# Performance work log

Measured on AMD Instinct MI355X. Metric: run time of the kernel, lower is better.

## Reference

```python
import jax, jax.numpy as jnp
import numpy as np

B, S, DIN, DOUT = 4, 4096, 4096, 4096
W_SCALE = 0.02  # kaiming-ish scale; keeps values inside fp8 range


def setup_inputs() -> dict:
    key = jax.random.key(0)
    k1, k2, k3 = jax.random.split(key, 3)
    x = jax.random.normal(k1, (B, S, DIN), dtype=jnp.float16)
    weight = (jax.random.normal(k2, (DOUT, DIN), dtype=jnp.float32) * W_SCALE).astype(jnp.float16)
    bias = (jax.random.normal(k3, (DOUT,), dtype=jnp.float32) * W_SCALE).astype(jnp.float16)
    return {"x": x, "weight": weight, "bias": bias}


def reference(x, weight, bias):
    # Emulate torch._scaled_mm: activations quantized to fp8 e5m2,
    # weight (transposed) quantized to fp8 e4m3fn, scale_a = scale_b = 1.0,
    # accumulate in fp32, add fp16 bias, output fp16.
    out_shape = x.shape[:-1] + (weight.shape[0],)
    x8 = x.reshape(-1, x.shape[-1]).astype(jnp.float8_e5m2)       # [M, DIN]
    w8 = weight.T.astype(jnp.float8_e4m3fn)                        # [DIN, DOUT]
    scale = jnp.float32(1.0)  # scale_a * scale_b
    acc = jnp.matmul(x8.astype(jnp.float32), w8.astype(jnp.float32))  # [M, DOUT] fp32 accum
    out = (acc * scale + bias.astype(jnp.float32)).astype(jnp.float16)
    return out.reshape(out_shape)
```

## Files before the change

### kernel.cpp

```cpp
#include <hip/hip_runtime.h>
#include <hip/hip_fp16.h>

#define M_DIM 16384
#define N_DIM 4096
#define K_DIM 4096

typedef __attribute__((ext_vector_type(16))) float f32x16;
typedef __attribute__((ext_vector_type(4)))  int   i32x4;
typedef __attribute__((ext_vector_type(8)))  int   i32x8;

template<bool E4M3>
__global__ __launch_bounds__(256) void quant_tile_kernel(
    const float* __restrict__ in,
    uint4* __restrict__ out,
    int ngrp)
{
  int t = blockIdx.x * 256 + threadIdx.x;
  if (t >= ngrp) return;
  const int g    = t & 1023;
  const int tile = t >> 10;
  const int kt   = tile & 63;
  const int bt   = tile >> 6;
  const int sb   = g >> 7;
  const int half = (g >> 6) & 1;
  const int l    = g & 63;
  const int row  = bt * 256 + sb * 32 + (l & 31);
  const int k    = kt * 64 + (l >> 5) * 32 + half * 16;

  const float4* p = reinterpret_cast<const float4*>(in + (size_t)row * K_DIM + k);
  float4 v0 = p[0], v1 = p[1], v2 = p[2], v3 = p[3];
  int w0 = 0, w1 = 0, w2 = 0, w3 = 0;
  if (E4M3) {
    w0 = __builtin_amdgcn_cvt_pk_fp8_f32(v0.x, v0.y, w0, false);
    w0 = __builtin_amdgcn_cvt_pk_fp8_f32(v0.z, v0.w, w0, true);
    w1 = __builtin_amdgcn_cvt_pk_fp8_f32(v1.x, v1.y, w1, false);
    w1 = __builtin_amdgcn_cvt_pk_fp8_f32(v1.z, v1.w, w1, true);
    w2 = __builtin_amdgcn_cvt_pk_fp8_f32(v2.x, v2.y, w2, false);
    w2 = __builtin_amdgcn_cvt_pk_fp8_f32(v2.z, v2.w, w2, true);
    w3 = __builtin_amdgcn_cvt_pk_fp8_f32(v3.x, v3.y, w3, false);
    w3 = __builtin_amdgcn_cvt_pk_fp8_f32(v3.z, v3.w, w3, true);
  } else {
    w0 = __builtin_amdgcn_cvt_pk_bf8_f32(v0.x, v0.y, w0, false);
    w0 = __builtin_amdgcn_cvt_pk_bf8_f32(v0.z, v0.w, w0, true);
    w1 = __builtin_amdgcn_cvt_pk_bf8_f32(v1.x, v1.y, w1, false);
    w1 = __builtin_amdgcn_cvt_pk_bf8_f32(v1.z, v1.w, w1, true);
    w2 = __builtin_amdgcn_cvt_pk_bf8_f32(v2.x, v2.y, w2, false);
    w2 = __builtin_amdgcn_cvt_pk_bf8_f32(v2.z, v2.w, w2, true);
    w3 = __builtin_amdgcn_cvt_pk_bf8_f32(v3.x, v3.y, w3, false);
    w3 = __builtin_amdgcn_cvt_pk_bf8_f32(v3.z, v3.w, w3, true);
  }
  out[t] = make_uint4((unsigned)w0, (unsigned)w1, (unsigned)w2, (unsigned)w3);
}

__global__ __launch_bounds__(512, 2) void gemm_fp8_kernel(
    const unsigned char* __restrict__ Aq,
    const unsigned char* __restrict__ Wq,
    const float* __restrict__ bias,
    float* __restrict__ C)
{
  __shared__ __align__(16) unsigned char lds[65536];

  const int tid  = threadIdx.x;
  const int lane = tid & 63;
  const int wave = tid >> 6;
  const int wr   = wave >> 2;
  const int wc   = wave & 3;

  const int bid = blockIdx.x;
  const int swz = (bid & 7) * 128 + (bid >> 3);
  const int bmi = swz >> 4;
  const int bni = swz & 15;

  const unsigned char* tA = Aq + (size_t)bmi * 64 * 16384;
  const unsigned char* tB = Wq + (size_t)bni * 64 * 16384;

  const size_t t16 = (size_t)tid * 16;
  const int    w1k = wave * 1024;

#define STAGE(gbase, ldsoff)                                                \
  __builtin_amdgcn_global_load_lds(                                         \
      (const __attribute__((address_space(1))) void*)((gbase) + t16),       \
      (__attribute__((address_space(3))) void*)(lds + (ldsoff) + w1k), 16, 0, 0)

#define RDFRAG(dst, byteoff)                                                \
  { const unsigned char* _p = lds + (byteoff) + lane * 16;                  \
    i32x4 _lo = *(const i32x4*)_p;                                          \
    i32x4 _hi = *(const i32x4*)(_p + 1024);                                 \
    dst = i32x8{_lo.x, _lo.y, _lo.z, _lo.w, _hi.x, _hi.y, _hi.z, _hi.w}; }

#define MFMA(d, a, b)                                                       \
  d = __builtin_amdgcn_mfma_scale_f32_32x32x64_f8f6f4(                      \
      a, b, d, 1 , 0 , 0, 0x7F7F7F7F, 0, 0x7F7F7F7F)

  const int aoff = wr * 8192;
  const int boff = 16384 + wc * 4096;

  f32x16 acc[4][2] = {};
  i32x8 aE0, aE1, aE2, aE3, bE0, bE1;
  i32x8 aO0, aO1, aO2, aO3, bO0, bO1;

  STAGE(tA,              0);
  STAGE(tA + 8192,       8192);
  STAGE(tB,              16384);
  STAGE(tB + 8192,       24576);
  __builtin_amdgcn_sched_barrier(0);
  STAGE(tA + 16384,          32768);
  STAGE(tA + 16384 + 8192,   40960);
  STAGE(tB + 16384,          49152);
  STAGE(tB + 16384 + 8192,   57344);
  __builtin_amdgcn_sched_barrier(0);
  asm volatile("s_waitcnt vmcnt(4)" ::: "memory");
  __builtin_amdgcn_s_barrier();
  RDFRAG(aE0, aoff + 0 * 2048);  RDFRAG(aE1, aoff + 1 * 2048);
  RDFRAG(aE2, aoff + 2 * 2048);  RDFRAG(aE3, aoff + 3 * 2048);
  RDFRAG(bE0, boff + 0 * 2048);  RDFRAG(bE1, boff + 1 * 2048);
  asm volatile("s_waitcnt lgkmcnt(0)" ::: "memory");
  __builtin_amdgcn_sched_barrier(0);
  __builtin_amdgcn_s_barrier();

  for (int kt = 0; kt < 64; kt += 2) {
    {
      const size_t tp = (size_t)((kt + 2) & 63) * 16384;
      STAGE(tA + tp,        0);
      STAGE(tA + tp + 8192, 8192);
      STAGE(tB + tp,        16384);
      STAGE(tB + tp + 8192, 24576);
      asm volatile("s_waitcnt vmcnt(4)" ::: "memory");
      __builtin_amdgcn_s_barrier();
      RDFRAG(aO0, 32768 + aoff + 0 * 2048);
      RDFRAG(aO1, 32768 + aoff + 1 * 2048);
      RDFRAG(aO2, 32768 + aoff + 2 * 2048);
      RDFRAG(aO3, 32768 + aoff + 3 * 2048);
      RDFRAG(bO0, 32768 + boff + 0 * 2048);
      RDFRAG(bO1, 32768 + boff + 1 * 2048);
      __builtin_amdgcn_s_setprio(1);
      MFMA(acc[0][0], aE0, bE0); MFMA(acc[0][1], aE0, bE1);
      MFMA(acc[1][0], aE1, bE0); MFMA(acc[1][1], aE1, bE1);
      MFMA(acc[2][0], aE2, bE0); MFMA(acc[2][1], aE2, bE1);
      MFMA(acc[3][0], aE3, bE0); MFMA(acc[3][1], aE3, bE1);
      __builtin_amdgcn_s_setprio(0);
      __builtin_amdgcn_sched_barrier(0);
      asm volatile("s_waitcnt lgkmcnt(0)" ::: "memory");
      __builtin_amdgcn_sched_barrier(0);
      __builtin_amdgcn_s_barrier();
    }
    {
      const size_t tp = (size_t)((kt + 3) & 63) * 16384;
      STAGE(tA + tp,        32768);
      STAGE(tA + tp + 8192, 40960);
      STAGE(tB + tp,        49152);
      STAGE(tB + tp + 8192, 57344);
      asm volatile("s_waitcnt vmcnt(4)" ::: "memory");
      __builtin_amdgcn_s_barrier();
      RDFRAG(aE0, aoff + 0 * 2048);
      RDFRAG(aE1, aoff + 1 * 2048);
      RDFRAG(aE2, aoff + 2 * 2048);
      RDFRAG(aE3, aoff + 3 * 2048);
      RDFRAG(bE0, boff + 0 * 2048);
      RDFRAG(bE1, boff + 1 * 2048);
      __builtin_amdgcn_s_setprio(1);
      MFMA(acc[0][0], aO0, bO0); MFMA(acc[0][1], aO0, bO1);
      MFMA(acc[1][0], aO1, bO0); MFMA(acc[1][1], aO1, bO1);
      MFMA(acc[2][0], aO2, bO0); MFMA(acc[2][1], aO2, bO1);
      MFMA(acc[3][0], aO3, bO0); MFMA(acc[3][1], aO3, bO1);
      __builtin_amdgcn_s_setprio(0);
      __builtin_amdgcn_sched_barrier(0);
      asm volatile("s_waitcnt lgkmcnt(0)" ::: "memory");
      __builtin_amdgcn_sched_barrier(0);
      __builtin_amdgcn_s_barrier();
    }
  }
#undef STAGE
#undef RDFRAG
#undef MFMA

  #pragma unroll
  for (int n = 0; n < 2; ++n) {
    const int col = bni * 256 + wc * 64 + n * 32 + (lane & 31);
    const float bv = bias[col];
    #pragma unroll
    for (int m = 0; m < 4; ++m) {
      const int rbase = bmi * 256 + wr * 128 + m * 32 + ((lane >> 5) << 2);
      #pragma unroll
      for (int r = 0; r < 16; ++r) {
        const int row = rbase + (r & 3) + 8 * (r >> 2);
        C[(size_t)row * N_DIM + col] =
            __half2float(__float2half_rn(acc[m][n][r] + bv));
      }
    }
  }
}

extern "C" void kernel_launch(void* const* d_in, const int* in_sizes, int n_in,
                              void* d_out, int out_size, void* d_ws, size_t ws_size,
                              hipStream_t stream) {
  const float* x  = (const float*)d_in[0];
  const float* w  = (const float*)d_in[1];
  const float* bs = (const float*)d_in[2];
  float* out = (float*)d_out;

  unsigned char* xq = (unsigned char*)d_ws;
  unsigned char* wq = (unsigned char*)d_ws + (size_t)M_DIM * K_DIM;

  const int ngx = (M_DIM * K_DIM) / 16;
  const int ngw = (N_DIM * K_DIM) / 16;
  quant_tile_kernel<false><<<ngx / 256, 256, 0, stream>>>(x, (uint4*)xq, ngx);
  quant_tile_kernel<true ><<<ngw / 256, 256, 0, stream>>>(w, (uint4*)wq, ngw);

  gemm_fp8_kernel<<<1024, 512, 0, stream>>>(xq, wq, bs, out);
}
```

Before: 358.2 us.

## Use 4 waves with 128x128 per-wave tiles and remap block order

Cuts the GEMM block from 8 waves to 4, so each wave computes a 128x128 sub-tile (4x4 MFMA accumulators) instead of 128x64. This raises register-level reuse of A/B fragments per LDS read. Each thread now issues 8 global-to-LDS loads per stage instead of 4. The block index mapping also changes so consecutive swizzled blocks walk along M within an N column rather than along N. The trade-off is fewer waves to hide latency and much higher register pressure (256 accumulator floats plus double-buffered fragments), with launch bounds of 1 block per CU.

```diff
diff --git a/kernel.cpp b/kernel.cpp
--- a/kernel.cpp
+++ b/kernel.cpp
@@ -52,7 +52,7 @@
   out[t] = make_uint4((unsigned)w0, (unsigned)w1, (unsigned)w2, (unsigned)w3);
 }
 
-__global__ __launch_bounds__(512, 2) void gemm_fp8_kernel(
+__global__ __launch_bounds__(256, 1) void gemm_fp8_kernel(
     const unsigned char* __restrict__ Aq,
     const unsigned char* __restrict__ Wq,
     const float* __restrict__ bias,
@@ -63,82 +63,94 @@
   const int tid  = threadIdx.x;
   const int lane = tid & 63;
   const int wave = tid >> 6;
-  const int wr   = wave >> 2;
-  const int wc   = wave & 3;
+  const int wr   = wave >> 1;
+  const int wc   = wave & 1;
 
   const int bid = blockIdx.x;
   const int swz = (bid & 7) * 128 + (bid >> 3);
-  const int bmi = swz >> 4;
-  const int bni = swz & 15;
-
-  const unsigned char* tA = Aq + (size_t)bmi * 64 * 16384;
-  const unsigned char* tB = Wq + (size_t)bni * 64 * 16384;
+  const int bni = swz >> 6;
+  const int bmi = swz & 63;
+
+  const unsigned char* tA = Aq + (size_t)bmi * (64 * 16384);
+  const unsigned char* tB = Wq + (size_t)bni * (64 * 16384);
 
   const size_t t16 = (size_t)tid * 16;
   const int    w1k = wave * 1024;
 
-#define STAGE(gbase, ldsoff)                                                \
-  __builtin_amdgcn_global_load_lds(                                         \
-      (const __attribute__((address_space(1))) void*)((gbase) + t16),       \
-      (__attribute__((address_space(3))) void*)(lds + (ldsoff) + w1k), 16, 0, 0)
-
-#define RDFRAG(dst, byteoff)                                                \
-  { const unsigned char* _p = lds + (byteoff) + lane * 16;                  \
-    i32x4 _lo = *(const i32x4*)_p;                                          \
-    i32x4 _hi = *(const i32x4*)(_p + 1024);                                 \
-    dst = i32x8{_lo.x, _lo.y, _lo.z, _lo.w, _hi.x, _hi.y, _hi.z, _hi.w}; }
-
-#define MFMA(d, a, b)                                                       \
-  d = __builtin_amdgcn_mfma_scale_f32_32x32x64_f8f6f4(                      \
-      a, b, d, 1 , 0 , 0, 0x7F7F7F7F, 0, 0x7F7F7F7F)
-
-  const int aoff = wr * 8192;
-  const int boff = 16384 + wc * 4096;
-
-  f32x16 acc[4][2] = {};
-  i32x8 aE0, aE1, aE2, aE3, bE0, bE1;
-  i32x8 aO0, aO1, aO2, aO3, bO0, bO1;
-
-  STAGE(tA,              0);
-  STAGE(tA + 8192,       8192);
-  STAGE(tB,              16384);
-  STAGE(tB + 8192,       24576);
+#define STAGE(gb, lo_)                                                      \
+  __builtin_amdgcn_global_load_lds(                                        \
+      (const __attribute__((address_space(1))) void*)((gb) + t16),          \
+      (__attribute__((address_space(3))) void*)(lds + (lo_) + w1k), 16, 0, 0)
+
+#define STAGE_TILE(tp, ldsbase)                                             \
+  STAGE(tA + (tp),         (ldsbase) + 0);                                  \
+  STAGE(tA + (tp) + 4096,  (ldsbase) + 4096);                               \
+  STAGE(tA + (tp) + 8192,  (ldsbase) + 8192);                               \
+  STAGE(tA + (tp) + 12288, (ldsbase) + 12288);                              \
+  STAGE(tB + (tp),         (ldsbase) + 16384);                              \
+  STAGE(tB + (tp) + 4096,  (ldsbase) + 20480);                              \
+  STAGE(tB + (tp) + 8192,  (ldsbase) + 24576);                              \
+  STAGE(tB + (tp) + 12288, (ldsbase) + 28672)
+
+#define RD(lo_, hi_, off)                                                   \
+  { const unsigned char* _p = lds + (off) + lane * 16;                      \
+    lo_ = *(const i32x4*)_p; hi_ = *(const i32x4*)(_p + 1024); }
+
+#define J(l_, h_) __builtin_shufflevector(l_, h_, 0, 1, 2, 3, 4, 5, 6, 7)
+
+  const int aoff = wr * 4 * 2048;
+  const int boff = 16384 + wc * 4 * 2048;
+
+  f32x16 acc[4][4] = {};
+  i32x4 aEl[4], aEh[4], bEl[4], bEh[4];
+  i32x4 aOl[4], aOh[4], bOl[4], bOh[4];
+
+  STAGE_TILE(0, 0);
   __builtin_amdgcn_sched_barrier(0);
-  STAGE(tA + 16384,          32768);
-  STAGE(tA + 16384 + 8192,   40960);
-  STAGE(tB + 16384,          49152);
-  STAGE(tB + 16384 + 8192,   57344);
+  STAGE_TILE(16384, 32768);
   __builtin_amdgcn_sched_barrier(0);
-  asm volatile("s_waitcnt vmcnt(4)" ::: "memory");
+  asm volatile("s_waitcnt vmcnt(8)" ::: "memory");
   __builtin_amdgcn_s_barrier();
-  RDFRAG(aE0, aoff + 0 * 2048);  RDFRAG(aE1, aoff + 1 * 2048);
-  RDFRAG(aE2, aoff + 2 * 2048);  RDFRAG(aE3, aoff + 3 * 2048);
-  RDFRAG(bE0, boff + 0 * 2048);  RDFRAG(bE1, boff + 1 * 2048);
+  #pragma unroll
+  for (int m = 0; m < 4; ++m) RD(aEl[m], aEh[m], aoff + m * 2048);
+  #pragma unroll
+  for (int n = 0; n < 4; ++n) RD(bEl[n], bEh[n], boff + n * 2048);
   asm volatile("s_waitcnt lgkmcnt(0)" ::: "memory");
   __builtin_amdgcn_sched_barrier(0);
   __builtin_amdgcn_s_barrier();
 
+#define CLUSTER(al, ah, bl, bh)                                             \
+  {                                                                         \
+    __builtin_amdgcn_s_setprio(1);                                          \
+    i32x8 B0 = J(bl[0], bh[0]), B1 = J(bl[1], bh[1]),                       \
+          B2 = J(bl[2], bh[2]), B3 = J(bl[3], bh[3]);                       \
+    _Pragma("unroll")                                                       \
+    for (int m = 0; m < 4; ++m) {                                           \
+      i32x8 Am = J(al[m], ah[m]);                                           \
+      acc[m][0] = __builtin_amdgcn_mfma_scale_f32_32x32x64_f8f6f4(          \
+          Am, B0, acc[m][0], 1, 0, 0, 0x7F7F7F7F, 0, 0x7F7F7F7F);           \
+      acc[m][1] = __builtin_amdgcn_mfma_scale_f32_32x32x64_f8f6f4(          \
+          Am, B1, acc[m][1], 1, 0, 0, 0x7F7F7F7F, 0, 0x7F7F7F7F);           \
+      acc[m][2] = __builtin_amdgcn_mfma_scale_f32_32x32x64_f8f6f4(          \
+          Am, B2, acc[m][2], 1, 0, 0, 0x7F7F7F7F, 0, 0x7F7F7F7F);           \
+      acc[m][3] = __builtin_amdgcn_mfma_scale_f32_32x32x64_f8f6f4(          \
+          Am, B3, acc[m][3], 1, 0, 0, 0x7F7F7F7F, 0, 0x7F7F7F7F);           \
+    }                                                                       \
+    __builtin_amdgcn_s_setprio(0);                                          \
+  }
+
   for (int kt = 0; kt < 64; kt += 2) {
     {
       const size_t tp = (size_t)((kt + 2) & 63) * 16384;
-      STAGE(tA + tp,        0);
-      STAGE(tA + tp + 8192, 8192);
-      STAGE(tB + tp,        16384);
-      STAGE(tB + tp + 8192, 24576);
-      asm volatile("s_waitcnt vmcnt(4)" ::: "memory");
-      __builtin_amdgcn_s_barrier();
-      RDFRAG(aO0, 32768 + aoff + 0 * 2048);
-      RDFRAG(aO1, 32768 + aoff + 1 * 2048);
-      RDFRAG(aO2, 32768 + aoff + 2 * 2048);
-      RDFRAG(aO3, 32768 + aoff + 3 * 2048);
-      RDFRAG(bO0, 32768 + boff + 0 * 2048);
-      RDFRAG(bO1, 32768 + boff + 1 * 2048);
-      __builtin_amdgcn_s_setprio(1);
-      MFMA(acc[0][0], aE0, bE0); MFMA(acc[0][1], aE0, bE1);
-      MFMA(acc[1][0], aE1, bE0); MFMA(acc[1][1], aE1, bE1);
-      MFMA(acc[2][0], aE2, bE0); MFMA(acc[2][1], aE2, bE1);
-      MFMA(acc[3][0], aE3, bE0); MFMA(acc[3][1], aE3, bE1);
-      __builtin_amdgcn_s_setprio(0);
+      STAGE_TILE(tp, 0);
+      asm volatile("s_waitcnt vmcnt(8)" ::: "memory");
+      __builtin_amdgcn_s_barrier();
+      #pragma unroll
+      for (int m = 0; m < 4; ++m) RD(aOl[m], aOh[m], 32768 + aoff + m * 2048);
+      #pragma unroll
+      for (int n = 0; n < 4; ++n) RD(bOl[n], bOh[n], 32768 + boff + n * 2048);
+      __builtin_amdgcn_sched_barrier(0);
+      CLUSTER(aEl, aEh, bEl, bEh);
       __builtin_amdgcn_sched_barrier(0);
       asm volatile("s_waitcnt lgkmcnt(0)" ::: "memory");
       __builtin_amdgcn_sched_barrier(0);
@@ -146,24 +158,15 @@
     }
     {
       const size_t tp = (size_t)((kt + 3) & 63) * 16384;
-      STAGE(tA + tp,        32768);
-      STAGE(tA + tp + 8192, 40960);
-      STAGE(tB + tp,        49152);
-      STAGE(tB + tp + 8192, 57344);
-      asm volatile("s_waitcnt vmcnt(4)" ::: "memory");
-      __builtin_amdgcn_s_barrier();
-      RDFRAG(aE0, aoff + 0 * 2048);
-      RDFRAG(aE1, aoff + 1 * 2048);
-      RDFRAG(aE2, aoff + 2 * 2048);
-      RDFRAG(aE3, aoff + 3 * 2048);
-      RDFRAG(bE0, boff + 0 * 2048);
-      RDFRAG(bE1, boff + 1 * 2048);
-      __builtin_amdgcn_s_setprio(1);
-      MFMA(acc[0][0], aO0, bO0); MFMA(acc[0][1], aO0, bO1);
-      MFMA(acc[1][0], aO1, bO0); MFMA(acc[1][1], aO1, bO1);
-      MFMA(acc[2][0], aO2, bO0); MFMA(acc[2][1], aO2, bO1);
-      MFMA(acc[3][0], aO3, bO0); MFMA(acc[3][1], aO3, bO1);
-      __builtin_amdgcn_s_setprio(0);
+      STAGE_TILE(tp, 32768);
+      asm volatile("s_waitcnt vmcnt(8)" ::: "memory");
+      __builtin_amdgcn_s_barrier();
+      #pragma unroll
+      for (int m = 0; m < 4; ++m) RD(aEl[m], aEh[m], aoff + m * 2048);
+      #pragma unroll
+      for (int n = 0; n < 4; ++n) RD(bEl[n], bEh[n], boff + n * 2048);
+      __builtin_amdgcn_sched_barrier(0);
+      CLUSTER(aOl, aOh, bOl, bOh);
       __builtin_amdgcn_sched_barrier(0);
       asm volatile("s_waitcnt lgkmcnt(0)" ::: "memory");
       __builtin_amdgcn_sched_barrier(0);
@@ -171,12 +174,14 @@
     }
   }
 #undef STAGE
-#undef RDFRAG
-#undef MFMA
+#undef STAGE_TILE
+#undef RD
+#undef J
+#undef CLUSTER
 
   #pragma unroll
-  for (int n = 0; n < 2; ++n) {
-    const int col = bni * 256 + wc * 64 + n * 32 + (lane & 31);
+  for (int n = 0; n < 4; ++n) {
+    const int col = bni * 256 + wc * 128 + n * 32 + (lane & 31);
     const float bv = bias[col];
     #pragma unroll
     for (int m = 0; m < 4; ++m) {
@@ -207,5 +212,5 @@
   quant_tile_kernel<false><<<ngx / 256, 256, 0, stream>>>(x, (uint4*)xq, ngx);
   quant_tile_kernel<true ><<<ngw / 256, 256, 0, stream>>>(w, (uint4*)wq, ngw);
 
-  gemm_fp8_kernel<<<1024, 512, 0, stream>>>(xq, wq, bs, out);
+  gemm_fp8_kernel<<<1024, 256, 0, stream>>>(xq, wq, bs, out);
 }
```

New measurement: 1.069 ms. 199% more time.
